# Kernel optimization log

Measured on AMD Instinct MI355X. Metric: run time of the kernel, lower is better.

The kernel has to match this reference:

```python
import jax, jax.numpy as jnp
import numpy as np

EPS = 1e-5
QB = 128.0  # 2**(bit-1), bit=8

def _int8_wrap(q):
    # Emulate torch's .to(torch.int8) two's-complement wrap (e.g. 128 -> -128).
    return jnp.mod(q + 128.0, 256.0) - 128.0

def setup_inputs() -> dict:
    key = jax.random.key(0)
    k1, k2, k3 = jax.random.split(key, 3)
    x = jax.random.normal(k1, (4, 2048, 2048), dtype=jnp.float32)
    weights = jax.random.normal(k2, (8192, 2048), dtype=jnp.float32)
    bias = jax.random.normal(k3, (8192,), dtype=jnp.float32)
    return {"x": x, "weights": weights, "bias": bias}

def reference(x, weights, bias):
    in_features = x.shape[-1]
    out_features = weights.shape[0]
    # LayerNorm over last dim, no affine (F.layer_norm defaults, eps=1e-5)
    mu = jnp.mean(x, axis=-1, keepdims=True)
    var = jnp.mean(jnp.square(x - mu), axis=-1, keepdims=True)
    input_norm = (x - mu) * jax.lax.rsqrt(var + EPS)
    # absmax int8 activation quant (nl_next=False path)
    max_val = jnp.max(jnp.abs(input_norm))
    q = _int8_wrap(jnp.round(input_norm * (QB / max_val)))
    dequant = max_val / QB
    # weight sign-binarization around the mean
    weight_quant = jnp.sign(weights - jnp.mean(weights))
    # quantized matmul + dequant scales + bias
    out = jnp.einsum('bsd,od->bso', q, weight_quant)  # [B,S,out]
    beta = jnp.sum(jnp.abs(weights)) / (in_features * out_features)
    out = out * (dequant * beta) + bias
    return out
```

## Files before the change

### kernel.cpp

```cpp
#include <hip/hip_runtime.h>


using i32x4 = __attribute__((ext_vector_type(4))) int;
using i32x16 = __attribute__((ext_vector_type(16))) int;

typedef const __attribute__((address_space(1))) void cg_void;
typedef __attribute__((address_space(3))) void lds_void;

#define K_DIM 2048
#define N_DIM 8192
#define M_DIM 8192
#define NELEM_W 16777216


__global__ __launch_bounds__(256) void pass1(const float* __restrict__ x,
                                             const float4* __restrict__ w4,
                                             float* __restrict__ mu_arr,
                                             float* __restrict__ rstd_arr,
                                             float* __restrict__ rowmax,
                                             double2* __restrict__ part) {
    __shared__ double sbd[8];
    __shared__ float sb1[4];
    __shared__ float sb2[8];
    const int bid = blockIdx.x, t = threadIdx.x;
    const int lane = t & 63, wv = t >> 6;
    if (bid < 1024) {
        double s = 0.0, a = 0.0;
        for (int i = bid * 256 + t; i < NELEM_W / 4; i += 1024 * 256) {
            float4 v = w4[i];
            s += (double)v.x + (double)v.y + (double)v.z + (double)v.w;
            a += fabs((double)v.x) + fabs((double)v.y) + fabs((double)v.z) + fabs((double)v.w);
        }
        for (int o = 32; o; o >>= 1) { s += __shfl_xor(s, o); a += __shfl_xor(a, o); }
        if (lane == 0) { sbd[wv] = s; sbd[4 + wv] = a; }
        __syncthreads();
        if (t == 0) {
            double2 r;
            r.x = sbd[0] + sbd[1] + sbd[2] + sbd[3];
            r.y = sbd[4] + sbd[5] + sbd[6] + sbd[7];
            part[bid] = r;
        }
    } else {
        const int row = bid - 1024;
        const float4* xr = (const float4*)x + (size_t)row * 512;
        float4 v0 = xr[t], v1 = xr[t + 256];
        float s = v0.x + v0.y + v0.z + v0.w + v1.x + v1.y + v1.z + v1.w;
        for (int o = 32; o; o >>= 1) s += __shfl_xor(s, o);
        if (lane == 0) sb1[wv] = s;
        __syncthreads();
        float mu = (sb1[0] + sb1[1] + sb1[2] + sb1[3]) * (1.0f / 2048.0f);
        float ssq = 0.f, md = 0.f, d;
        d = v0.x - mu; ssq += d * d; md = fmaxf(md, fabsf(d));
        d = v0.y - mu; ssq += d * d; md = fmaxf(md, fabsf(d));
        d = v0.z - mu; ssq += d * d; md = fmaxf(md, fabsf(d));
        d = v0.w - mu; ssq += d * d; md = fmaxf(md, fabsf(d));
        d = v1.x - mu; ssq += d * d; md = fmaxf(md, fabsf(d));
        d = v1.y - mu; ssq += d * d; md = fmaxf(md, fabsf(d));
        d = v1.z - mu; ssq += d * d; md = fmaxf(md, fabsf(d));
        d = v1.w - mu; ssq += d * d; md = fmaxf(md, fabsf(d));
        for (int o = 32; o; o >>= 1) {
            ssq += __shfl_xor(ssq, o);
            md = fmaxf(md, __shfl_xor(md, o));
        }
        if (lane == 0) { sb2[wv] = ssq; sb2[4 + wv] = md; }
        __syncthreads();
        if (t == 0) {
            float var = (sb2[0] + sb2[1] + sb2[2] + sb2[3]) * (1.0f / 2048.0f);
            float rstd = 1.0f / sqrtf(var + 1e-5f);
            mu_arr[row] = mu;
            rstd_arr[row] = rstd;
            rowmax[row] = fmaxf(fmaxf(sb2[4], sb2[5]), fmaxf(sb2[6], sb2[7])) * rstd;
        }
    }
}

__global__ __launch_bounds__(256) void wred2(const double2* __restrict__ part,
                                             const float* __restrict__ rowmax,
                                             unsigned* __restrict__ scal) {
    double s = 0.0, a = 0.0;
    float m = 0.f;
    const int t = threadIdx.x, lane = t & 63, wv = t >> 6;
    for (int i = t; i < 1024; i += 256) { double2 p = part[i]; s += p.x; a += p.y; }
    for (int i = t; i < 8192; i += 256) m = fmaxf(m, rowmax[i]);
    for (int o = 32; o; o >>= 1) {
        s += __shfl_xor(s, o); a += __shfl_xor(a, o);
        m = fmaxf(m, __shfl_xor(m, o));
    }
    __shared__ double sbd[8];
    __shared__ float sbm[4];
    if (lane == 0) { sbd[wv] = s; sbd[4 + wv] = a; sbm[wv] = m; }
    __syncthreads();
    if (t == 0) {
        double st = sbd[0] + sbd[1] + sbd[2] + sbd[3];
        double at = sbd[4] + sbd[5] + sbd[6] + sbd[7];
        ((float*)scal)[0] = fmaxf(fmaxf(sbm[0], sbm[1]), fmaxf(sbm[2], sbm[3]));
        ((float*)scal)[1] = (float)(st / (double)NELEM_W);
        ((float*)scal)[2] = (float)(at / (double)NELEM_W);
    }
}

__device__ __forceinline__ int sgn8(float d) { return (d > 0.f) ? 1 : ((d < 0.f) ? -1 : 0); }

__global__ __launch_bounds__(256) void pass2(const float* __restrict__ x,
                                             const float4* __restrict__ w4,
                                             const float* __restrict__ mu_arr,
                                             const float* __restrict__ rstd_arr,
                                             const unsigned* __restrict__ scal,
                                             signed char* __restrict__ q,
                                             int4* __restrict__ wq4) {
    const int bid = blockIdx.x, t = threadIdx.x;
    if (bid < 1024) {
        float wm = ((const float*)scal)[1];
        for (int i = bid * 256 + t; i < NELEM_W / 16; i += 1024 * 256) {
            int words[4];
            #pragma unroll
            for (int jj = 0; jj < 4; ++jj) {
                float4 v = w4[i * 4 + jj];
                int b0 = sgn8(v.x - wm) & 255, b1 = sgn8(v.y - wm) & 255;
                int b2 = sgn8(v.z - wm) & 255, b3 = sgn8(v.w - wm) & 255;
                words[jj] = b0 | (b1 << 8) | (b2 << 16) | (b3 << 24);
            }
            wq4[i] = make_int4(words[0], words[1], words[2], words[3]);
        }
    } else {
        const int row = bid - 1024;
        float mu = mu_arr[row], rstd = rstd_arr[row];
        float s = 128.0f / ((const float*)scal)[0];
        const float4* xr = (const float4*)x + (size_t)row * 512;
        float4 v0 = xr[2 * t], v1 = xr[2 * t + 1];
        float xs[8] = {v0.x, v0.y, v0.z, v0.w, v1.x, v1.y, v1.z, v1.w};
        int b[8];
        #pragma unroll
        for (int j = 0; j < 8; ++j) {
            float norm = (xs[j] - mu) * rstd;
            int qi = (int)rintf(norm * s);
            b[j] = qi & 255;
        }
        int w0 = b[0] | (b[1] << 8) | (b[2] << 16) | (b[3] << 24);
        int w1 = b[4] | (b[5] << 8) | (b[6] << 16) | (b[7] << 24);
        ((int2*)(q + (size_t)row * 2048))[t] = make_int2(w0, w1);
    }
}

#define LD16(p) (*(const i32x4*)(p))
#define TB 32768

#define STAGE(koff, sbase)                                                                  \
    do {                                                                                    \
        __builtin_amdgcn_global_load_lds((cg_void*)(gA + (koff)),                           \
            (lds_void*)(lds + (sbase) + w * 2048), 16, 0, 0);                               \
        __builtin_amdgcn_global_load_lds((cg_void*)(gA + 16 * K_DIM + (koff)),              \
            (lds_void*)(lds + (sbase) + w * 2048 + 1024), 16, 0, 0);                        \
        __builtin_amdgcn_global_load_lds((cg_void*)(gB + (koff)),                           \
            (lds_void*)(lds + (sbase) + 16384 + w * 2048), 16, 0, 0);                       \
        __builtin_amdgcn_global_load_lds((cg_void*)(gB + 16 * K_DIM + (koff)),              \
            (lds_void*)(lds + (sbase) + 16384 + w * 2048 + 1024), 16, 0, 0);                \
    } while (0)

__global__ __launch_bounds__(512, 2) void gemm_i8(const signed char* __restrict__ A,
                                                  const signed char* __restrict__ B,
                                                  const float* __restrict__ bias,
                                                  const unsigned* __restrict__ scal,
                                                  float* __restrict__ C) {
    __shared__ alignas(16) char lds[65536];
    const int t = threadIdx.x, w = t >> 6, lane = t & 63;

    const int wg = blockIdx.x;
    const int xcd = wg & 7, idx = wg >> 3;
    const int bm = (xcd * 4 + (idx >> 5)) * 256;
    const int bn = (idx & 31) * 256;

    const int wr = w >> 2, wc = w & 3;
    const int r32 = lane & 31, hi = lane >> 5;

    const int srow = lane >> 2;
    const int scol = ((lane & 3) ^ ((lane >> 3) & 3)) << 4;
    const signed char* gA = A + (size_t)(bm + w * 32 + srow) * K_DIM + scol;
    const signed char* gB = B + (size_t)(bn + w * 32 + srow) * K_DIM + scol;

    const char* aBase = lds + (wr * 128 + r32) * 64;
    const char* bBase = lds + 16384 + (wc * 64 + r32) * 64;
    const int swz = ((r32 >> 1) & 3) << 4;
    const int sw0 = (hi * 16) ^ swz;
    const int sw1 = (32 + hi * 16) ^ swz;

    const float scale = (((const float*)scal)[0] * (1.0f / 128.0f)) * ((const float*)scal)[2];

    i32x16 acc[4][2] = {};
    i32x4 a0[4], a1[4], b0[2], b1[2];

    STAGE(0, 0);

    for (int kt = 0; kt < 32; ++kt) {
        const int c = (kt & 1) * TB;
        if (kt < 31) {
            STAGE((kt + 1) * 64, ((kt + 1) & 1) * TB);
            asm volatile("s_waitcnt vmcnt(4)" ::: "memory");
        } else {
            asm volatile("s_waitcnt vmcnt(0)" ::: "memory");
        }
        __builtin_amdgcn_s_barrier();

        #pragma unroll
        for (int mb = 0; mb < 4; ++mb) a0[mb] = LD16(aBase + c + mb * 2048 + sw0);
        #pragma unroll
        for (int nb = 0; nb < 2; ++nb) b0[nb] = LD16(bBase + c + nb * 2048 + sw0);
        #pragma unroll
        for (int mb = 0; mb < 4; ++mb) a1[mb] = LD16(aBase + c + mb * 2048 + sw1);
        #pragma unroll
        for (int nb = 0; nb < 2; ++nb) b1[nb] = LD16(bBase + c + nb * 2048 + sw1);
        __builtin_amdgcn_s_setprio(1);
        #pragma unroll
        for (int mb = 0; mb < 4; ++mb)
            #pragma unroll
            for (int nb = 0; nb < 2; ++nb)
                acc[mb][nb] = __builtin_amdgcn_mfma_i32_32x32x32_i8(a0[mb], b0[nb],
                                                                    acc[mb][nb], 0, 0, 0);
        #pragma unroll
        for (int mb = 0; mb < 4; ++mb)
            #pragma unroll
            for (int nb = 0; nb < 2; ++nb)
                acc[mb][nb] = __builtin_amdgcn_mfma_i32_32x32x32_i8(a1[mb], b1[nb],
                                                                    acc[mb][nb], 0, 0, 0);
        __builtin_amdgcn_s_setprio(0);
        __builtin_amdgcn_s_barrier();
    }

    const int colbase = bn + wc * 64;
    float bi[2];
    #pragma unroll
    for (int nb = 0; nb < 2; ++nb) bi[nb] = bias[colbase + nb * 32 + r32];
    #pragma unroll
    for (int mb = 0; mb < 4; ++mb) {
        #pragma unroll
        for (int nb = 0; nb < 2; ++nb) {
            #pragma unroll
            for (int r = 0; r < 16; ++r) {
                int row = bm + wr * 128 + mb * 32 + (r & 3) + 8 * (r >> 2) + 4 * hi;
                int col = colbase + nb * 32 + r32;
                C[(size_t)row * N_DIM + col] = (float)acc[mb][nb][r] * scale + bi[nb];
            }
        }
    }
}

extern "C" void kernel_launch(void* const* d_in, const int* in_sizes, int n_in,
                              void* d_out, int out_size, void* d_ws, size_t ws_size,
                              hipStream_t stream) {
    const float* x = (const float*)d_in[0];
    const float* wts = (const float*)d_in[1];
    const float* bias = (const float*)d_in[2];
    float* out = (float*)d_out;

    char* ws = (char*)d_ws;
    unsigned* scal = (unsigned*)ws;
    double2* part = (double2*)(ws + 1024);
    float* mu = (float*)(ws + 32768);
    float* rstd = (float*)(ws + 65536);
    float* rowmax = (float*)(ws + 98304);
    signed char* q = (signed char*)(ws + 131072);
    signed char* wq = (signed char*)(ws + 131072 + 16777216);

    hipLaunchKernelGGL(pass1, dim3(9216), dim3(256), 0, stream,
                       x, (const float4*)wts, mu, rstd, rowmax, part);
    hipLaunchKernelGGL(wred2, dim3(1), dim3(256), 0, stream, part, rowmax, scal);
    hipLaunchKernelGGL(pass2, dim3(9216), dim3(256), 0, stream,
                       x, (const float4*)wts, mu, rstd, scal, q, (int4*)wq);
    hipLaunchKernelGGL(gemm_i8, dim3(1024), dim3(512), 0, stream,
                       q, wq, bias, scal, out);
}
```

Baseline: 236.4 us.

## Switch int8 GEMM to 16x16x64 MFMA with four-slab LDS pipeline

Replaces the 32x32x32 int8 MFMA tiles with 16x16x64 MFMAs and grows LDS from two to four 32KB slabs, prefetching up to three K-slabs ahead. The main loop now interleaves fragment loads, global-to-LDS slab issues and MFMA clusters in four phases per iteration, each separated by barriers. The aim is to hide global latency behind more compute and to use a denser MFMA shape. In exchange the kernel needs 128KB of LDS per block, which likely allows only one block per CU despite launch_bounds(512,2), and adds many more barriers per iteration.

```diff
diff --git a/kernel.cpp b/kernel.cpp
--- a/kernel.cpp
+++ b/kernel.cpp
@@ -2,7 +2,6 @@
 
 
 using i32x4 = __attribute__((ext_vector_type(4))) int;
-using i32x16 = __attribute__((ext_vector_type(16))) int;
 
 typedef const __attribute__((address_space(1))) void cg_void;
 typedef __attribute__((address_space(3))) void lds_void;
@@ -143,26 +142,38 @@
 }
 
 #define LD16(p) (*(const i32x4*)(p))
-#define TB 32768
-
-#define STAGE(koff, sbase)                                                                  \
+
+#define ISSUE_SLAB(s)                                                                       \
     do {                                                                                    \
-        __builtin_amdgcn_global_load_lds((cg_void*)(gA + (koff)),                           \
-            (lds_void*)(lds + (sbase) + w * 2048), 16, 0, 0);                               \
-        __builtin_amdgcn_global_load_lds((cg_void*)(gA + 16 * K_DIM + (koff)),              \
-            (lds_void*)(lds + (sbase) + w * 2048 + 1024), 16, 0, 0);                        \
-        __builtin_amdgcn_global_load_lds((cg_void*)(gB + (koff)),                           \
-            (lds_void*)(lds + (sbase) + 16384 + w * 2048), 16, 0, 0);                       \
-        __builtin_amdgcn_global_load_lds((cg_void*)(gB + 16 * K_DIM + (koff)),              \
-            (lds_void*)(lds + (sbase) + 16384 + w * 2048 + 1024), 16, 0, 0);                \
+        const int bb_ = ((s) & 3) * 32768;                                                  \
+        const int ko_ = ((s) >> 1) * 128 + ((s) & 1) * 64;                                  \
+        __builtin_amdgcn_global_load_lds((cg_void*)(gA + ko_),                              \
+            (lds_void*)(lds + bb_ + w * 2048), 16, 0, 0);                                   \
+        __builtin_amdgcn_global_load_lds((cg_void*)(gA + 16 * K_DIM + ko_),                 \
+            (lds_void*)(lds + bb_ + w * 2048 + 1024), 16, 0, 0);                            \
+        __builtin_amdgcn_global_load_lds((cg_void*)(gB + ko_),                              \
+            (lds_void*)(lds + bb_ + 16384 + w * 2048), 16, 0, 0);                           \
+        __builtin_amdgcn_global_load_lds((cg_void*)(gB + 16 * K_DIM + ko_),                 \
+            (lds_void*)(lds + bb_ + 16384 + w * 2048 + 1024), 16, 0, 0);                    \
     } while (0)
+
+#define MF16(MB, AF, BF)                                                                    \
+    __builtin_amdgcn_s_setprio(1);                                                          \
+    _Pragma("unroll") for (int mm = 0; mm < 4; ++mm)                                        \
+        _Pragma("unroll") for (int nn = 0; nn < 4; ++nn)                                    \
+            acc[(MB) + mm][nn] = __builtin_amdgcn_mfma_i32_16x16x64_i8(                     \
+                AF[mm], BF[nn], acc[(MB) + mm][nn], 0, 0, 0);                               \
+    __builtin_amdgcn_s_setprio(0);
+
+#define BAR() __builtin_amdgcn_s_barrier()
+#define LGKM0() asm volatile("s_waitcnt lgkmcnt(0)" ::: "memory")
 
 __global__ __launch_bounds__(512, 2) void gemm_i8(const signed char* __restrict__ A,
                                                   const signed char* __restrict__ B,
                                                   const float* __restrict__ bias,
                                                   const unsigned* __restrict__ scal,
                                                   float* __restrict__ C) {
-    __shared__ alignas(16) char lds[65536];
+    __shared__ alignas(16) char lds[131072];
     const int t = threadIdx.x, w = t >> 6, lane = t & 63;
 
     const int wg = blockIdx.x;
@@ -171,73 +182,83 @@
     const int bn = (idx & 31) * 256;
 
     const int wr = w >> 2, wc = w & 3;
-    const int r32 = lane & 31, hi = lane >> 5;
+    const int r16 = lane & 15, ko = lane >> 4;
 
     const int srow = lane >> 2;
     const int scol = ((lane & 3) ^ ((lane >> 3) & 3)) << 4;
     const signed char* gA = A + (size_t)(bm + w * 32 + srow) * K_DIM + scol;
     const signed char* gB = B + (size_t)(bn + w * 32 + srow) * K_DIM + scol;
 
-    const char* aBase = lds + (wr * 128 + r32) * 64;
-    const char* bBase = lds + 16384 + (wc * 64 + r32) * 64;
-    const int swz = ((r32 >> 1) & 3) << 4;
-    const int sw0 = (hi * 16) ^ swz;
-    const int sw1 = (32 + hi * 16) ^ swz;
+    const char* aBase = lds + (wr * 128 + r16) * 64;
+    const char* bBase = lds + 16384 + (wc * 64 + r16) * 64;
+    const int sw = (ko * 16) ^ (((r16 >> 1) & 3) << 4);
 
     const float scale = (((const float*)scal)[0] * (1.0f / 128.0f)) * ((const float*)scal)[2];
 
-    i32x16 acc[4][2] = {};
-    i32x4 a0[4], a1[4], b0[2], b1[2];
-
-    STAGE(0, 0);
-
-    for (int kt = 0; kt < 32; ++kt) {
-        const int c = (kt & 1) * TB;
-        if (kt < 31) {
-            STAGE((kt + 1) * 64, ((kt + 1) & 1) * TB);
-            asm volatile("s_waitcnt vmcnt(4)" ::: "memory");
-        } else {
-            asm volatile("s_waitcnt vmcnt(0)" ::: "memory");
-        }
-        __builtin_amdgcn_s_barrier();
-
-        #pragma unroll
-        for (int mb = 0; mb < 4; ++mb) a0[mb] = LD16(aBase + c + mb * 2048 + sw0);
-        #pragma unroll
-        for (int nb = 0; nb < 2; ++nb) b0[nb] = LD16(bBase + c + nb * 2048 + sw0);
-        #pragma unroll
-        for (int mb = 0; mb < 4; ++mb) a1[mb] = LD16(aBase + c + mb * 2048 + sw1);
-        #pragma unroll
-        for (int nb = 0; nb < 2; ++nb) b1[nb] = LD16(bBase + c + nb * 2048 + sw1);
-        __builtin_amdgcn_s_setprio(1);
-        #pragma unroll
-        for (int mb = 0; mb < 4; ++mb)
+    i32x4 acc[8][4] = {};
+    i32x4 a0[4], a1[4], b0[4], b1[4];
+
+    ISSUE_SLAB(0);
+    ISSUE_SLAB(1);
+    ISSUE_SLAB(2);
+    asm volatile("s_waitcnt vmcnt(8)" ::: "memory");
+    BAR();
+
+    for (int kt = 0; kt < 16; ++kt) {
+        const int c0 = ((2 * kt) & 3) * 32768;
+        const int c1 = ((2 * kt + 1) & 3) * 32768;
+
+        #pragma unroll
+        for (int mb = 0; mb < 4; ++mb) a0[mb] = LD16(aBase + c0 + mb * 1024 + sw);
+        #pragma unroll
+        for (int nb = 0; nb < 4; ++nb) b0[nb] = LD16(bBase + c0 + nb * 1024 + sw);
+        if (kt == 15) asm volatile("s_waitcnt vmcnt(0)" ::: "memory");
+        else          asm volatile("s_waitcnt vmcnt(4)" ::: "memory");
+        BAR();
+        LGKM0();
+        MF16(0, a0, b0);
+        BAR();
+
+        if (kt <= 14) ISSUE_SLAB(2 * kt + 3);
+        #pragma unroll
+        for (int mb = 0; mb < 4; ++mb) a1[mb] = LD16(aBase + c1 + mb * 1024 + sw);
+        #pragma unroll
+        for (int nb = 0; nb < 4; ++nb) b1[nb] = LD16(bBase + c1 + nb * 1024 + sw);
+        BAR();
+        LGKM0();
+        MF16(0, a1, b1);
+        BAR();
+
+        #pragma unroll
+        for (int mb = 0; mb < 4; ++mb) a0[mb] = LD16(aBase + c0 + (4 + mb) * 1024 + sw);
+        BAR();
+        LGKM0();
+        MF16(4, a0, b0);
+        BAR();
+
+        if (kt <= 13) ISSUE_SLAB(2 * kt + 4);
+        #pragma unroll
+        for (int mb = 0; mb < 4; ++mb) a1[mb] = LD16(aBase + c1 + (4 + mb) * 1024 + sw);
+        if (kt <= 13)      asm volatile("s_waitcnt vmcnt(8)" ::: "memory");
+        else if (kt == 14) asm volatile("s_waitcnt vmcnt(4)" ::: "memory");
+        BAR();
+        LGKM0();
+        MF16(4, a1, b1);
+        BAR();
+    }
+
+    const int colbase = bn + wc * 64;
+    float bi[4];
+    #pragma unroll
+    for (int nb = 0; nb < 4; ++nb) bi[nb] = bias[colbase + nb * 16 + r16];
+    #pragma unroll
+    for (int mb = 0; mb < 8; ++mb) {
+        #pragma unroll
+        for (int nb = 0; nb < 4; ++nb) {
             #pragma unroll
-            for (int nb = 0; nb < 2; ++nb)
-                acc[mb][nb] = __builtin_amdgcn_mfma_i32_32x32x32_i8(a0[mb], b0[nb],
-                                                                    acc[mb][nb], 0, 0, 0);
-        #pragma unroll
-        for (int mb = 0; mb < 4; ++mb)
-            #pragma unroll
-            for (int nb = 0; nb < 2; ++nb)
-                acc[mb][nb] = __builtin_amdgcn_mfma_i32_32x32x32_i8(a1[mb], b1[nb],
-                                                                    acc[mb][nb], 0, 0, 0);
-        __builtin_amdgcn_s_setprio(0);
-        __builtin_amdgcn_s_barrier();
-    }
-
-    const int colbase = bn + wc * 64;
-    float bi[2];
-    #pragma unroll
-    for (int nb = 0; nb < 2; ++nb) bi[nb] = bias[colbase + nb * 32 + r32];
-    #pragma unroll
-    for (int mb = 0; mb < 4; ++mb) {
-        #pragma unroll
-        for (int nb = 0; nb < 2; ++nb) {
-            #pragma unroll
-            for (int r = 0; r < 16; ++r) {
-                int row = bm + wr * 128 + mb * 32 + (r & 3) + 8 * (r >> 2) + 4 * hi;
-                int col = colbase + nb * 32 + r32;
+            for (int r = 0; r < 4; ++r) {
+                int row = bm + wr * 128 + mb * 16 + ko * 4 + r;
+                int col = colbase + nb * 16 + r16;
                 C[(size_t)row * N_DIM + col] = (float)acc[mb][nb][r] * scale + bi[nb];
             }
         }
```

Result: no change. 232.4 us (-1.7%).
